# Optimization experiments

Hardware: AMD Instinct MI355X
Metric: run time of the kernel (lower is better)

Reference implementation:

```python
import jax, jax.numpy as jnp
import numpy as np

NINP, NC, NH = 34, 128, 512
B, S, T = 64, 2048, 400
EPS = 1e-10


def _lstm_cell(x, h, c, Wih, Whh, bih, bhh):
    # torch.nn.LSTMCell gate order: i, f, g, o
    g = x @ Wih.T + bih + h @ Whh.T + bhh
    i, f, gg, o = jnp.split(g, 4, axis=1)
    c2 = jax.nn.sigmoid(f) * c + jax.nn.sigmoid(i) * jnp.tanh(gg)
    h2 = jax.nn.sigmoid(o) * jnp.tanh(c2)
    return h2, c2


def _attend(keys, values, mask, query):
    # energy: [B, S]; mask: [B, S] float 0/1
    energy = jnp.einsum('bc,bsc->bs', query, keys) * mask
    energy = energy - (1.0 - mask) * 1e6
    e = jnp.exp(energy - energy.max(axis=1, keepdims=True)) * mask
    att = e / e.sum(axis=1, keepdims=True)
    ctx = jnp.einsum('bs,bsc->bc', att, values)
    return att, ctx


def setup_inputs() -> dict:
    key = jax.random.key(0)
    ks = jax.random.split(key, 32)
    def rn(k, shape, scale=0.05):
        return (jax.random.normal(k, shape) * scale).astype(jnp.float32)
    inp = {
        'keys': rn(ks[0], (B, S, NC), 1.0),
        'values': rn(ks[1], (B, S, NC), 1.0),
        'lens': jax.random.randint(ks[2], (B,), S // 2, S + 1),
        'inputs': jax.random.randint(ks[3], (B, T), 0, NINP),
        'emb': rn(ks[4], (NINP, NC)),
        'wq': rn(ks[5], (NC, NH)), 'bq': jnp.zeros((NC,), jnp.float32),
        'wc': rn(ks[6], (NC, NH + NC)), 'bc': jnp.zeros((NC,), jnp.float32),
        'b_out': jnp.zeros((NINP,), jnp.float32),
    }
    in_sizes = [2 * NC, NH, NH]
    for l in range(3):
        inp['w%d_ih' % l] = rn(ks[7 + 4 * l], (4 * NH, in_sizes[l]))
        inp['w%d_hh' % l] = rn(ks[8 + 4 * l], (4 * NH, NH))
        inp['b%d_ih' % l] = jnp.zeros((4 * NH,), jnp.float32)
        inp['b%d_hh' % l] = jnp.zeros((4 * NH,), jnp.float32)
        inp['h0_%d' % l] = jnp.zeros((NH,), jnp.float32)  # ALSTMCell h0 param (zero init)
        inp['c0_%d' % l] = jnp.zeros((NH,), jnp.float32)
    return inp


def reference(keys, values, lens, inputs, emb, wq, bq, wc, bc, b_out,
              w0_ih, w0_hh, b0_ih, b0_hh, h0_0, c0_0,
              w1_ih, w1_hh, b1_ih, b1_hh, h0_1, c0_1,
              w2_ih, w2_hh, b2_ih, b2_hh, h0_2, c0_2):
    mask = (jnp.arange(S)[None, :] < lens[:, None]).astype(keys.dtype)  # [B,S]
    h1 = jnp.broadcast_to(h0_0[None], (B, NH)); c1 = jnp.broadcast_to(c0_0[None], (B, NH))
    h2 = jnp.broadcast_to(h0_1[None], (B, NH)); c2 = jnp.broadcast_to(c0_1[None], (B, NH))
    h3 = jnp.broadcast_to(h0_2[None], (B, NH)); c3 = jnp.broadcast_to(c0_2[None], (B, NH))
    # initial attention from last layer's h0 (matches torch forward)
    query0 = h3 @ wq.T + bq
    _, ctx = _attend(keys, values, mask, query0)
    # precompute gumbel noise for all T steps: -log(eps - log(U + eps))
    U = jax.random.uniform(jax.random.key(1), (T, B, NINP), dtype=jnp.float32)
    gnoise = -jnp.log(EPS - jnp.log(U + EPS))

    def step(carry, xs):
        h1, c1, h2, c2, h3, c3, ctx = carry
        tok, gn = xs
        x = jnp.concatenate([emb[tok], ctx], axis=1)  # [B, 2*NC]
        h1, c1 = _lstm_cell(x, h1, c1, w0_ih, w0_hh, b0_ih, b0_hh)
        h2, c2 = _lstm_cell(h1, h2, c2, w1_ih, w1_hh, b1_ih, b1_hh)
        h3, c3 = _lstm_cell(h2, h3, c3, w2_ih, w2_hh, b2_ih, b2_hh)
        q = h3 @ wq.T + bq
        att, ctx = _attend(keys, values, mask, q)
        z = jax.nn.leaky_relu(jnp.concatenate([h3, ctx], axis=1) @ wc.T + bc, 0.01)
        logit = z @ emb.T + b_out  # tied output weight = embedding
        gen = jnp.argmax(logit + gn, axis=1)
        return (h1, c1, h2, c2, h3, c3, ctx), (logit, att, gen)

    _, (logits, attentions, generated) = jax.lax.scan(
        step, (h1, c1, h2, c2, h3, c3, ctx), (inputs.T, gnoise))
    return logits, attentions, generated
```

## Files before the change

kernel.cpp:

```cpp
#include <hip/hip_runtime.h>

#define NINP 34
#define NCC  128
#define NHH  512
#define BBB  64
#define SSS  2048
#define TTT  400
#define GEPS 1e-10f

#define GDIM 512
#define NTHR 256
#define NCHK 8
#define SCHK 256

#define JAX_PARTITIONABLE 1

#define OFF_H   0
#define OFF_C   196608
#define OFF_CTX 294912
#define OFF_ML  303104
#define OFF_P   303616

#define SY_ROOT 0
#define SY_GEN  16
#define SY_LEAFC(l) (256 + 8 * (l))
#define SY_LEAFG(l) (512 + 8 * (l))
#define SY_BF(b)    (1024 + 8 * (b))
#define SY_MF(b)    (1536 + 8 * (b))

struct Params {
  const float* keys; const float* values;
  const int* lens;  const int* toks;
  const float* emb; const float* wq; const float* bq;
  const float* wc;  const float* bc; const float* bout;
  const float* wih[3]; const float* whh[3];
  const float* bih[3]; const float* bhh[3];
  const float* h0[3];  const float* c0[3];
  float* out_logits; float* out_att; float* out_gen;
  float* wsf; unsigned* sync;
};

__device__ __forceinline__ float4 ld4(const float* p) { return *(const float4*)p; }
__device__ __forceinline__ float sigf(float x) { return 1.0f / (1.0f + expf(-x)); }

__device__ __forceinline__ unsigned aload(const unsigned* p) {
  return __hip_atomic_load(p, __ATOMIC_RELAXED, __HIP_MEMORY_SCOPE_AGENT);
}
__device__ __forceinline__ unsigned aadd(unsigned* p, unsigned v) {
  return __hip_atomic_fetch_add(p, v, __ATOMIC_RELAXED, __HIP_MEMORY_SCOPE_AGENT);
}
__device__ __forceinline__ void astore(unsigned* p, unsigned v) {
  __hip_atomic_store(p, v, __ATOMIC_RELAXED, __HIP_MEMORY_SCOPE_AGENT);
}
__device__ __forceinline__ float ldc(const float* p) {
  unsigned u = __hip_atomic_load((const unsigned*)p, __ATOMIC_RELAXED, __HIP_MEMORY_SCOPE_AGENT);
  return __uint_as_float(u);
}
__device__ __forceinline__ void stc(float* p, float v) {
  __hip_atomic_store((unsigned*)p, __float_as_uint(v), __ATOMIC_RELAXED, __HIP_MEMORY_SCOPE_AGENT);
}
__device__ __forceinline__ float4 ld4c(const float* p) {
  unsigned long long a = __hip_atomic_load((const unsigned long long*)p,
                                           __ATOMIC_RELAXED, __HIP_MEMORY_SCOPE_AGENT);
  unsigned long long b = __hip_atomic_load(((const unsigned long long*)p) + 1,
                                           __ATOMIC_RELAXED, __HIP_MEMORY_SCOPE_AGENT);
  float4 r;
  r.x = __uint_as_float((unsigned)a); r.y = __uint_as_float((unsigned)(a >> 32));
  r.z = __uint_as_float((unsigned)b); r.w = __uint_as_float((unsigned)(b >> 32));
  return r;
}
__device__ __forceinline__ void wait_vm0() {
  asm volatile("s_waitcnt vmcnt(0)" ::: "memory");
}
__device__ __forceinline__ void cbar() { asm volatile("" ::: "memory"); }

__device__ void gbar(unsigned* sync, unsigned& epoch, int bid) {
  wait_vm0();
  __syncthreads();
  if (threadIdx.x == 0) {
    epoch++;
    const int leaf = bid >> 4;
    const bool leader = (bid & 15) == 0;
    if (aadd(&sync[SY_LEAFC(leaf)], 1u) == 16u * epoch - 1u) {
      if (aadd(&sync[SY_ROOT], 1u) == 32u * epoch - 1u)
        astore(&sync[SY_GEN], epoch);
    }
    if (leader) {
      while (aload(&sync[SY_GEN]) < epoch) __builtin_amdgcn_s_sleep(1);
      astore(&sync[SY_LEAFG(leaf)], epoch);
    } else {
      while (aload(&sync[SY_LEAFG(leaf)]) < epoch) __builtin_amdgcn_s_sleep(1);
    }
  }
  __syncthreads();
  cbar();
}

__device__ __forceinline__ void waitflag(unsigned* p, unsigned target) {
  if (threadIdx.x == 0) {
    while (aload(p) < target) __builtin_amdgcn_s_sleep(2);
  }
  __syncthreads();
  cbar();
}
__device__ __forceinline__ void postflag(unsigned* p) {
  wait_vm0();
  __syncthreads();
  if (threadIdx.x == 0) aadd(p, 1u);
}

__device__ __forceinline__ void tfr(unsigned& x0, unsigned& x1, int r) {
  x0 += x1; x1 = (x1 << r) | (x1 >> (32 - r)); x1 ^= x0;
}
__device__ unsigned threefry_bits(unsigned idx) {
  const unsigned k0 = 0u, k1 = 1u;
  const unsigned k2 = 0x1BD11BDAu ^ k0 ^ k1;
#if JAX_PARTITIONABLE
  unsigned x0 = 0u, x1 = idx;
#else
  const unsigned half = (TTT * BBB * NINP) / 2;
  const bool lo = idx < half;
  unsigned x0 = lo ? idx : idx - half;
  unsigned x1 = lo ? idx + half : idx;
#endif
  x0 += k0; x1 += k1;
  tfr(x0,x1,13); tfr(x0,x1,15); tfr(x0,x1,26); tfr(x0,x1,6);
  x0 += k1; x1 += k2 + 1u;
  tfr(x0,x1,17); tfr(x0,x1,29); tfr(x0,x1,16); tfr(x0,x1,24);
  x0 += k2; x1 += k0 + 2u;
  tfr(x0,x1,13); tfr(x0,x1,15); tfr(x0,x1,26); tfr(x0,x1,6);
  x0 += k0; x1 += k1 + 3u;
  tfr(x0,x1,17); tfr(x0,x1,29); tfr(x0,x1,16); tfr(x0,x1,24);
  x0 += k1; x1 += k2 + 4u;
  tfr(x0,x1,13); tfr(x0,x1,15); tfr(x0,x1,26); tfr(x0,x1,6);
  x0 += k2; x1 += k0 + 5u;
#if JAX_PARTITIONABLE
  return x0 ^ x1;
#else
  return lo ? x0 : x1;
#endif
}
__device__ __forceinline__ float gumbel(unsigned idx) {
  unsigned bits = threefry_bits(idx);
  float u = __uint_as_float((bits >> 9) | 0x3f800000u) - 1.0f;
  u = fmaxf(u, 0.0f);
  return -logf(GEPS - logf(u + GEPS));
}

template<int L>
__device__ void lstm_layer(const Params& p, int t, const float* hin, float* hout,
                           float* sh, int ug, int boct, int tid) {
  const float* hin_l = hin + L * BBB * NHH + (size_t)boct * 8 * NHH;
  float* houtl = hout + L * BBB * NHH;
  float* cl = p.wsf + OFF_C + L * BBB * NHH;
  const float* xlow = (L == 0) ? (const float*)0
                               : (hout + (L - 1) * BBB * NHH + (size_t)boct * 8 * NHH);

  const int insz = (L == 0) ? (2 * NCC) : NHH;
  const int nx = insz >> 7;
  const int nch = nx + 4;

  const int rhat = tid >> 3;
  const int bloc = tid & 7;
  const int g = rhat >> 3, jl = rhat & 7;
  const int j = ug * 8 + jl;
  const int row = g * NHH + j;
  const float* wr  = p.wih[L] + (size_t)row * insz;
  const float* wr2 = p.whh[L] + (size_t)row * NHH;

  float* xb0 = sh;
  float* xb1 = sh + 1056;
  const int kk  = (tid & 31) << 2;
  const int rb0 = tid >> 5;

  float4 pf;
  auto issue = [&](int cc) {
    const int rb = rb0;
    const int gb = boct * 8 + rb;
    const bool isx = cc < nx;
    const int off = (isx ? cc : cc - nx) << 7;
    if (L == 0) {
      if (isx) pf = (cc == 0)
          ? ld4(p.emb + (size_t)p.toks[gb * TTT + t] * NCC + kk)
          : ld4c(p.wsf + OFF_CTX + gb * NCC + kk);
      else pf = ld4c(hin_l + (size_t)rb * NHH + off + kk);
    } else {
      pf = isx ? ld4c(xlow + (size_t)rb * NHH + off + kk)
               : ld4c(hin_l + (size_t)rb * NHH + off + kk);
    }
  };
  auto commit = [&](float* buf) {
    *(float4*)&buf[rb0 * 132 + kk] = pf;
  };

  float acc = p.bih[L][row] + p.bhh[L][row];
  float s0 = 0.f, s1 = 0.f, s2 = 0.f, s3 = 0.f;

  issue(0);
  commit(xb0);
  __syncthreads();
  for (int cc = 0; cc < nch; ++cc) {
    if (cc + 1 < nch) issue(cc + 1);
    const bool isx = cc < nx;
    const int off = (isx ? cc : cc - nx) << 7;
    const float* wp = (isx ? wr : wr2) + off;
    const float* xr = ((cc & 1) ? xb1 : xb0) + bloc * 132;
#pragma unroll 8
    for (int k = 0; k < 128; k += 4) {
      float4 w = ld4(wp + k);
      float4 x = ld4(xr + k);
      s0 = fmaf(w.x, x.x, s0); s1 = fmaf(w.y, x.y, s1);
      s2 = fmaf(w.z, x.z, s2); s3 = fmaf(w.w, x.w, s3);
    }
    if (cc + 1 < nch) commit((cc & 1) ? xb0 : xb1);
    __syncthreads();
  }
  acc += (s0 + s1) + (s2 + s3);

  float* gl = sh + 2112;
  gl[rhat * 8 + bloc] = acc;
  __syncthreads();
  if (tid < 64) {
    const int jl2 = tid >> 3, bl = tid & 7;
    const int b = boct * 8 + bl;
    const int jj = ug * 8 + jl2;
    const float iv = gl[(0  + jl2) * 8 + bl];
    const float fv = gl[(8  + jl2) * 8 + bl];
    const float gv = gl[(16 + jl2) * 8 + bl];
    const float ov = gl[(24 + jl2) * 8 + bl];
    const float cold = cl[(size_t)b * NHH + jj];
    const float cnew = sigf(fv) * cold + sigf(iv) * tanhf(gv);
    const float hnew = sigf(ov) * tanhf(cnew);
    cl[(size_t)b * NHH + jj] = cnew;
    stc(&houtl[(size_t)b * NHH + jj], hnew);
  }
}

__device__ void attend_phase(const Params& p, int a, int t, const float* h3,
                             float* sh, int bid, int tid, bool wout) {
  float* wsf = p.wsf;
  unsigned* sync = p.sync;
  const int b  = (bid & 7) * 8 + (bid >> 6);
  const int ch = (bid >> 3) & 7;
  const int sbase = ch * SCHK;

  float* us  = sh + 8704;
  float* qs  = sh + 9344;
  float* ps  = sh + 9472;
  float* red = sh + 9728;
  float* zs  = sh + 10784;
  float* lg  = sh + 10912;

  if (tid < 128) *(float4*)&us[tid * 4] = ld4c(h3 + (size_t)b * NHH + tid * 4);
  __syncthreads();
  if (tid < NCC) {
    const float* wr = p.wq + (size_t)tid * NHH;
    float s0 = 0.f, s1 = 0.f, s2 = 0.f, s3 = 0.f;
#pragma unroll 8
    for (int k = 0; k < NHH; k += 4) {
      float4 w = ld4(wr + k);
      s0 = fmaf(w.x, us[k],     s0); s1 = fmaf(w.y, us[k + 1], s1);
      s2 = fmaf(w.z, us[k + 2], s2); s3 = fmaf(w.w, us[k + 3], s3);
    }
    qs[tid] = p.bq[tid] + (s0 + s1) + (s2 + s3);
  }
  const int lenb = p.lens[b];
  __syncthreads();

  const int s = sbase + tid;
  const bool msk = s < lenb;
  float e = -1e6f;
  if (msk) {
    const float* kr = p.keys + ((size_t)b * SSS + s) * NCC;
    float e0 = 0.f, e1 = 0.f, e2 = 0.f, e3 = 0.f;
#pragma unroll 8
    for (int c = 0; c < NCC; c += 4) {
      float4 kv = ld4(kr + c);
      e0 = fmaf(qs[c],     kv.x, e0); e1 = fmaf(qs[c + 1], kv.y, e1);
      e2 = fmaf(qs[c + 2], kv.z, e2); e3 = fmaf(qs[c + 3], kv.w, e3);
    }
    e = (e0 + e1) + (e2 + e3);
  }

  float mx = e;
#pragma unroll
  for (int off = 32; off; off >>= 1) mx = fmaxf(mx, __shfl_xor(mx, off));
  if ((tid & 63) == 0) red[tid >> 6] = mx;
  __syncthreads();
  const float mc = fmaxf(fmaxf(red[0], red[1]), fmaxf(red[2], red[3]));
  const float pv = msk ? expf(e - mc) : 0.f;
  ps[tid] = pv;
  float ls = pv;
#pragma unroll
  for (int off = 32; off; off >>= 1) ls += __shfl_xor(ls, off);
  if ((tid & 63) == 0) red[4 + (tid >> 6)] = ls;
  __syncthreads();
  const float lc = (red[4] + red[5]) + (red[6] + red[7]);

  const int c4 = (tid & 31) << 2;
  const int sg = tid >> 5;
  float r0 = 0.f, r1 = 0.f, r2 = 0.f, r3 = 0.f;
  const int nval = min(max(lenb - sbase - sg * 32, 0), 32);
  const float* vb = p.values + ((size_t)b * SSS + sbase + sg * 32) * NCC + c4;
#pragma unroll 4
  for (int i2 = 0; i2 < nval; ++i2) {
    const float pw = ps[sg * 32 + i2];
    float4 vv = ld4(vb + (size_t)i2 * NCC);
    r0 = fmaf(pw, vv.x, r0); r1 = fmaf(pw, vv.y, r1);
    r2 = fmaf(pw, vv.z, r2); r3 = fmaf(pw, vv.w, r3);
  }
  __syncthreads();
  *(float4*)&red[sg * 132 + c4] = make_float4(r0, r1, r2, r3);
  __syncthreads();
  float* pout = wsf + OFF_P + ((size_t)b * NCHK + ch) * 132;
  if (tid < NCC) {
    float sum = 0.f;
#pragma unroll
    for (int sg2 = 0; sg2 < 8; ++sg2) sum += red[sg2 * 132 + tid];
    stc(&pout[2 + tid], sum);
  }
  if (tid == 0) { stc(&pout[0], mc); stc(&pout[1], lc); }
  postflag(&sync[SY_BF(b)]);

  float gm = 0.f, gL = 1.f;
  if (ch == 0) {
    waitflag(&sync[SY_BF(b)], (unsigned)(NCHK * (a + 1)));
    const float* pb = wsf + OFF_P + (size_t)b * NCHK * 132;
    if (tid < 8)       red[tid] = ldc(&pb[tid * 132]);
    else if (tid < 16) red[tid] = ldc(&pb[(tid - 8) * 132 + 1]);
    __syncthreads();
    float m = red[0];
#pragma unroll
    for (int i = 1; i < 8; ++i) m = fmaxf(m, red[i]);
    float L = 0.f;
#pragma unroll
    for (int i = 0; i < 8; ++i) L += red[8 + i] * expf(red[i] - m);
    gm = m; gL = L;
    if (tid < NCC) {
      float v = 0.f;
#pragma unroll
      for (int c2 = 0; c2 < NCHK; ++c2)
        v += ldc(&pb[c2 * 132 + 2 + tid]) * expf(red[c2] - m);
      v /= L;
      stc(&wsf[OFF_CTX + b * NCC + tid], v);
      us[NHH + tid] = v;
    }
    if (tid == 0) { stc(&wsf[OFF_ML + b * 8], m); stc(&wsf[OFF_ML + b * 8 + 1], L); }
    postflag(&sync[SY_MF(b)]);
  } else if (wout) {
    waitflag(&sync[SY_MF(b)], (unsigned)(a + 1));
    gm = ldc(&wsf[OFF_ML + b * 8]);
    gL = ldc(&wsf[OFF_ML + b * 8 + 1]);
  }

  if (wout) {
    float* ao = p.out_att + ((size_t)t * BBB + b) * SSS;
    ao[s] = (msk ? expf(e - gm) : 0.f) / gL;
    if (ch == 0) {
      if (tid < NCC) {
        const float* wr = p.wc + (size_t)tid * (NHH + NCC);
        float s0 = 0.f, s1 = 0.f, s2 = 0.f, s3 = 0.f;
#pragma unroll 8
        for (int k = 0; k < NHH + NCC; k += 4) {
          float4 w = ld4(wr + k);
          s0 = fmaf(w.x, us[k],     s0); s1 = fmaf(w.y, us[k + 1], s1);
          s2 = fmaf(w.z, us[k + 2], s2); s3 = fmaf(w.w, us[k + 3], s3);
        }
        float z = (s0 + s1) + (s2 + s3) + p.bc[tid];
        zs[tid] = (z >= 0.f) ? z : 0.01f * z;
      }
      __syncthreads();
      if (tid < NINP) {
        const float* er = p.emb + tid * NCC;
        float s0 = 0.f, s1 = 0.f, s2 = 0.f, s3 = 0.f;
#pragma unroll 8
        for (int k = 0; k < NCC; k += 4) {
          float4 w = ld4(er + k);
          s0 = fmaf(w.x, zs[k],     s0); s1 = fmaf(w.y, zs[k + 1], s1);
          s2 = fmaf(w.z, zs[k + 2], s2); s3 = fmaf(w.w, zs[k + 3], s3);
        }
        const float lgt = (s0 + s1) + (s2 + s3) + p.bout[tid];
        p.out_logits[((size_t)t * BBB + b) * NINP + tid] = lgt;
        lg[tid] = lgt + gumbel((unsigned)(t * (BBB * NINP) + b * NINP + tid));
      }
      __syncthreads();
      if (tid == 0) {
        float bv = lg[0]; int bix = 0;
        for (int i = 1; i < NINP; ++i) if (lg[i] > bv) { bv = lg[i]; bix = i; }
        p.out_gen[t * BBB + b] = (float)bix;
      }
      __syncthreads();
    }
  }
}

extern "C" __global__ void __launch_bounds__(NTHR, 2)
decoder_kernel(Params p) {
  __shared__ float sh[11008];
  const int bid = blockIdx.x;
  const int tid = threadIdx.x;
  const int ug   = (bid & 7) * 8 + ((bid >> 3) & 7);
  const int boct = bid >> 6;
  unsigned epoch = 0;
  unsigned* sync = p.sync;
  float* wsf = p.wsf;

  if (tid < 192) {
    const int l = tid >> 6, u = tid & 63;
    const int jl = u >> 3, bl = u & 7;
    const int b = boct * 8 + bl;
    const int j = ug * 8 + jl;
    stc(&wsf[OFF_H + ((size_t)l * BBB + b) * NHH + j], p.h0[l][j]);
    wsf[OFF_C + ((size_t)l * BBB + b) * NHH + j] = p.c0[l][j];
  }
  gbar(sync, epoch, bid);

  attend_phase(p, 0, -1, wsf + OFF_H + 2 * BBB * NHH, sh, bid, tid, false);
  gbar(sync, epoch, bid);

  for (int t = 0; t < TTT; ++t) {
    const float* hin = wsf + OFF_H + ((t & 1) ? 3 * BBB * NHH : 0);
    float* hout      = wsf + OFF_H + ((t & 1) ? 0 : 3 * BBB * NHH);

    lstm_layer<0>(p, t, hin, hout, sh, ug, boct, tid);
    gbar(sync, epoch, bid);
    lstm_layer<1>(p, t, hin, hout, sh, ug, boct, tid);
    gbar(sync, epoch, bid);
    lstm_layer<2>(p, t, hin, hout, sh, ug, boct, tid);
    gbar(sync, epoch, bid);
    attend_phase(p, t + 1, t, hout + 2 * BBB * NHH, sh, bid, tid, true);
    gbar(sync, epoch, bid);
  }
}

extern "C" void kernel_launch(void* const* d_in, const int* in_sizes, int n_in,
                              void* d_out, int out_size, void* d_ws, size_t ws_size,
                              hipStream_t stream) {
  Params p;
  p.keys   = (const float*)d_in[0];
  p.values = (const float*)d_in[1];
  p.lens   = (const int*)d_in[2];
  p.toks   = (const int*)d_in[3];
  p.emb    = (const float*)d_in[4];
  p.wq     = (const float*)d_in[5];
  p.bq     = (const float*)d_in[6];
  p.wc     = (const float*)d_in[7];
  p.bc     = (const float*)d_in[8];
  p.bout   = (const float*)d_in[9];
  for (int l = 0; l < 3; ++l) {
    p.wih[l] = (const float*)d_in[10 + 6 * l];
    p.whh[l] = (const float*)d_in[11 + 6 * l];
    p.bih[l] = (const float*)d_in[12 + 6 * l];
    p.bhh[l] = (const float*)d_in[13 + 6 * l];
    p.h0[l]  = (const float*)d_in[14 + 6 * l];
    p.c0[l]  = (const float*)d_in[15 + 6 * l];
  }
  float* out = (float*)d_out;
  p.out_logits = out;
  p.out_att    = out + (size_t)TTT * BBB * NINP;
  p.out_gen    = out + (size_t)TTT * BBB * NINP + (size_t)TTT * BBB * SSS;
  p.sync = (unsigned*)d_ws;
  p.wsf  = (float*)((char*)d_ws + 8192);

  hipMemsetAsync(d_ws, 0, 8192, stream);
  decoder_kernel<<<dim3(GDIM), dim3(NTHR), 0, stream>>>(p);
}
```

Measured before the change: 43.23 ms.

## Precompute recurrent Whh·h partials off the critical path of LSTM layers

Restructures the per-step schedule so each layer's recurrent product Whh·h(t) is computed as soon as h is produced. Layer L+1 reuses its staged input to also compute Whh[L]·h_L, and the attention phase computes Whh[2]·h3 plus the next token's embedding term. This shrinks the serialized work between grid barriers: layer 0 does only the ctx part, and layers 1 and 2 do a single shared input pass. The h buffers are no longer double-buffered, and the attention chunk assignment is rotated, adding register state and extra work in the attention phase.

```diff
diff --git a/kernel.cpp b/kernel.cpp
--- a/kernel.cpp
+++ b/kernel.cpp
@@ -147,75 +147,126 @@
   return -logf(GEPS - logf(u + GEPS));
 }
 
+__device__ float pc_dot_h(const float* hsrc, const float* wrow, float* sh, int tid) {
+  float* xb0 = sh;
+  const int kk = (tid & 31) << 2;
+  const int rb0 = tid >> 5;
+  const int bloc = tid & 7;
+  float s0 = 0.f, s1 = 0.f, s2 = 0.f, s3 = 0.f;
+  for (int cc = 0; cc < 4; ++cc) {
+    __syncthreads();
+    *(float4*)&xb0[rb0 * 132 + kk] = ld4c(hsrc + (size_t)rb0 * NHH + (cc << 7) + kk);
+    __syncthreads();
+    const float* xr = xb0 + bloc * 132;
+    const float* wp = wrow + (cc << 7);
+#pragma unroll 8
+    for (int k = 0; k < 128; k += 4) {
+      float4 w = ld4(wp + k);
+      float4 x = ld4(xr + k);
+      s0 = fmaf(w.x, x.x, s0); s1 = fmaf(w.y, x.y, s1);
+      s2 = fmaf(w.z, x.z, s2); s3 = fmaf(w.w, x.w, s3);
+    }
+  }
+  return (s0 + s1) + (s2 + s3);
+}
+
+__device__ float pc_dot_emb(const Params& p, int tnext, const float* wrow,
+                            float* sh, int boct, int tid) {
+  float* xb0 = sh;
+  const int kk = (tid & 31) << 2;
+  const int rb0 = tid >> 5;
+  const int bloc = tid & 7;
+  const int gb = boct * 8 + rb0;
+  __syncthreads();
+  *(float4*)&xb0[rb0 * 132 + kk] =
+      ld4(p.emb + (size_t)p.toks[gb * TTT + tnext] * NCC + kk);
+  __syncthreads();
+  const float* xr = xb0 + bloc * 132;
+  float s0 = 0.f, s1 = 0.f, s2 = 0.f, s3 = 0.f;
+#pragma unroll 8
+  for (int k = 0; k < 128; k += 4) {
+    float4 w = ld4(wrow + k);
+    float4 x = ld4(xr + k);
+    s0 = fmaf(w.x, x.x, s0); s1 = fmaf(w.y, x.y, s1);
+    s2 = fmaf(w.z, x.z, s2); s3 = fmaf(w.w, x.w, s3);
+  }
+  return (s0 + s1) + (s2 + s3);
+}
+
 template<int L>
-__device__ void lstm_layer(const Params& p, int t, const float* hin, float* hout,
-                           float* sh, int ug, int boct, int tid) {
-  const float* hin_l = hin + L * BBB * NHH + (size_t)boct * 8 * NHH;
+__device__ void lstm_layer(const Params& p, float* hout, float* sh, int ug, int boct,
+                           int tid, float use_hacc, float embacc, float* prod_hacc) {
   float* houtl = hout + L * BBB * NHH;
   float* cl = p.wsf + OFF_C + L * BBB * NHH;
-  const float* xlow = (L == 0) ? (const float*)0
+  const float* xsrc = (L == 0) ? (const float*)0
                                : (hout + (L - 1) * BBB * NHH + (size_t)boct * 8 * NHH);
-
-  const int insz = (L == 0) ? (2 * NCC) : NHH;
-  const int nx = insz >> 7;
-  const int nch = nx + 4;
 
   const int rhat = tid >> 3;
   const int bloc = tid & 7;
   const int g = rhat >> 3, jl = rhat & 7;
   const int j = ug * 8 + jl;
   const int row = g * NHH + j;
-  const float* wr  = p.wih[L] + (size_t)row * insz;
-  const float* wr2 = p.whh[L] + (size_t)row * NHH;
+  constexpr int insz = (L == 0) ? (2 * NCC) : NHH;
+  const float* wx = p.wih[L] + (size_t)row * insz + ((L == 0) ? NCC : 0);
+  const float* wh = (L == 0) ? (const float*)0 : (p.whh[L - 1] + (size_t)row * NHH);
 
   float* xb0 = sh;
   float* xb1 = sh + 1056;
-  const int kk  = (tid & 31) << 2;
+  const int kk = (tid & 31) << 2;
   const int rb0 = tid >> 5;
+  const int gb = boct * 8 + rb0;
+  constexpr int nch = (L == 0) ? 1 : 4;
+
+  float xs0 = 0.f, xs1 = 0.f, xs2 = 0.f, xs3 = 0.f;
+  float hs0 = 0.f, hs1 = 0.f, hs2 = 0.f, hs3 = 0.f;
 
   float4 pf;
   auto issue = [&](int cc) {
-    const int rb = rb0;
-    const int gb = boct * 8 + rb;
-    const bool isx = cc < nx;
-    const int off = (isx ? cc : cc - nx) << 7;
-    if (L == 0) {
-      if (isx) pf = (cc == 0)
-          ? ld4(p.emb + (size_t)p.toks[gb * TTT + t] * NCC + kk)
-          : ld4c(p.wsf + OFF_CTX + gb * NCC + kk);
-      else pf = ld4c(hin_l + (size_t)rb * NHH + off + kk);
+    if constexpr (L == 0) {
+      (void)cc;
+      pf = ld4c(p.wsf + OFF_CTX + gb * NCC + kk);
     } else {
-      pf = isx ? ld4c(xlow + (size_t)rb * NHH + off + kk)
-               : ld4c(hin_l + (size_t)rb * NHH + off + kk);
+      pf = ld4c(xsrc + (size_t)rb0 * NHH + (cc << 7) + kk);
     }
   };
-  auto commit = [&](float* buf) {
-    *(float4*)&buf[rb0 * 132 + kk] = pf;
-  };
-
-  float acc = p.bih[L][row] + p.bhh[L][row];
-  float s0 = 0.f, s1 = 0.f, s2 = 0.f, s3 = 0.f;
+  auto commit = [&](float* buf) { *(float4*)&buf[rb0 * 132 + kk] = pf; };
 
   issue(0);
   commit(xb0);
   __syncthreads();
   for (int cc = 0; cc < nch; ++cc) {
     if (cc + 1 < nch) issue(cc + 1);
-    const bool isx = cc < nx;
-    const int off = (isx ? cc : cc - nx) << 7;
-    const float* wp = (isx ? wr : wr2) + off;
+    const int off = cc << 7;
     const float* xr = ((cc & 1) ? xb1 : xb0) + bloc * 132;
-#pragma unroll 8
-    for (int k = 0; k < 128; k += 4) {
-      float4 w = ld4(wp + k);
-      float4 x = ld4(xr + k);
-      s0 = fmaf(w.x, x.x, s0); s1 = fmaf(w.y, x.y, s1);
-      s2 = fmaf(w.z, x.z, s2); s3 = fmaf(w.w, x.w, s3);
+    const float* wp = wx + off;
+    if constexpr (L == 0) {
+#pragma unroll 8
+      for (int k = 0; k < 128; k += 4) {
+        float4 w = ld4(wp + k);
+        float4 x = ld4(xr + k);
+        xs0 = fmaf(w.x, x.x, xs0); xs1 = fmaf(w.y, x.y, xs1);
+        xs2 = fmaf(w.z, x.z, xs2); xs3 = fmaf(w.w, x.w, xs3);
+      }
+    } else {
+      const float* wp2 = wh + off;
+#pragma unroll 8
+      for (int k = 0; k < 128; k += 4) {
+        float4 x = ld4(xr + k);
+        float4 w = ld4(wp + k);
+        xs0 = fmaf(w.x, x.x, xs0); xs1 = fmaf(w.y, x.y, xs1);
+        xs2 = fmaf(w.z, x.z, xs2); xs3 = fmaf(w.w, x.w, xs3);
+        float4 w2 = ld4(wp2 + k);
+        hs0 = fmaf(w2.x, x.x, hs0); hs1 = fmaf(w2.y, x.y, hs1);
+        hs2 = fmaf(w2.z, x.z, hs2); hs3 = fmaf(w2.w, x.w, hs3);
+      }
     }
     if (cc + 1 < nch) commit((cc & 1) ? xb0 : xb1);
     __syncthreads();
   }
-  acc += (s0 + s1) + (s2 + s3);
+  if constexpr (L > 0) *prod_hacc = (hs0 + hs1) + (hs2 + hs3);
+
+  float acc = p.bih[L][row] + p.bhh[L][row] + (xs0 + xs1) + (xs2 + xs3) + use_hacc;
+  if constexpr (L == 0) acc += embacc;
 
   float* gl = sh + 2112;
   gl[rhat * 8 + bloc] = acc;
@@ -237,12 +288,13 @@
 }
 
 __device__ void attend_phase(const Params& p, int a, int t, const float* h3,
-                             float* sh, int bid, int tid, bool wout) {
+                             float* sh, int bid, int tid, bool wout,
+                             int ug, int boct, int pc_t, float* hacc2, float* embacc) {
   float* wsf = p.wsf;
   unsigned* sync = p.sync;
   const int b  = (bid & 7) * 8 + (bid >> 6);
   const int ch = (bid >> 3) & 7;
-  const int sbase = ch * SCHK;
+  const int sbase = ((ch + 7) & 7) * SCHK;
 
   float* us  = sh + 8704;
   float* qs  = sh + 9344;
@@ -322,7 +374,11 @@
   if (tid == 0) { stc(&pout[0], mc); stc(&pout[1], lc); }
   postflag(&sync[SY_BF(b)]);
 
-  float gm = 0.f, gL = 1.f;
+  const int rowp = ((tid >> 3) >> 3) * NHH + (ug * 8 + ((tid >> 3) & 7));
+  const float* wh2row = p.whh[2] + (size_t)rowp * NHH;
+  const float* w0row  = p.wih[0] + (size_t)rowp * (2 * NCC);
+  const float* h3pc   = p.wsf + OFF_H + 2 * BBB * NHH + (size_t)boct * 8 * NHH;
+
   if (ch == 0) {
     waitflag(&sync[SY_BF(b)], (unsigned)(NCHK * (a + 1)));
     const float* pb = wsf + OFF_P + (size_t)b * NCHK * 132;
@@ -335,7 +391,6 @@
     float L = 0.f;
 #pragma unroll
     for (int i = 0; i < 8; ++i) L += red[8 + i] * expf(red[i] - m);
-    gm = m; gL = L;
     if (tid < NCC) {
       float v = 0.f;
 #pragma unroll
@@ -347,16 +402,14 @@
     }
     if (tid == 0) { stc(&wsf[OFF_ML + b * 8], m); stc(&wsf[OFF_ML + b * 8 + 1], L); }
     postflag(&sync[SY_MF(b)]);
-  } else if (wout) {
-    waitflag(&sync[SY_MF(b)], (unsigned)(a + 1));
-    gm = ldc(&wsf[OFF_ML + b * 8]);
-    gL = ldc(&wsf[OFF_ML + b * 8 + 1]);
-  }
-
-  if (wout) {
-    float* ao = p.out_att + ((size_t)t * BBB + b) * SSS;
-    ao[s] = (msk ? expf(e - gm) : 0.f) / gL;
-    if (ch == 0) {
+
+    if (pc_t >= 0) {
+      *hacc2  = pc_dot_h(h3pc, wh2row, sh, tid);
+      *embacc = pc_dot_emb(p, pc_t, w0row, sh, boct, tid);
+    }
+    if (wout) {
+      float* ao = p.out_att + ((size_t)t * BBB + b) * SSS;
+      ao[s] = (msk ? expf(e - m) : 0.f) / L;
       if (tid < NCC) {
         const float* wr = p.wc + (size_t)tid * (NHH + NCC);
         float s0 = 0.f, s1 = 0.f, s2 = 0.f, s3 = 0.f;
@@ -391,6 +444,18 @@
       }
       __syncthreads();
     }
+  } else {
+    if (pc_t >= 0) {
+      *hacc2  = pc_dot_h(h3pc, wh2row, sh, tid);
+      *embacc = pc_dot_emb(p, pc_t, w0row, sh, boct, tid);
+    }
+    if (wout) {
+      waitflag(&sync[SY_MF(b)], (unsigned)(a + 1));
+      const float gm = ldc(&wsf[OFF_ML + b * 8]);
+      const float gL = ldc(&wsf[OFF_ML + b * 8 + 1]);
+      float* ao = p.out_att + ((size_t)t * BBB + b) * SSS;
+      ao[s] = (msk ? expf(e - gm) : 0.f) / gL;
+    }
   }
 }
 
@@ -404,31 +469,43 @@
   unsigned epoch = 0;
   unsigned* sync = p.sync;
   float* wsf = p.wsf;
+  float* hbuf = wsf + OFF_H;
 
   if (tid < 192) {
     const int l = tid >> 6, u = tid & 63;
     const int jl = u >> 3, bl = u & 7;
     const int b = boct * 8 + bl;
     const int j = ug * 8 + jl;
-    stc(&wsf[OFF_H + ((size_t)l * BBB + b) * NHH + j], p.h0[l][j]);
+    stc(&hbuf[((size_t)l * BBB + b) * NHH + j], p.h0[l][j]);
     wsf[OFF_C + ((size_t)l * BBB + b) * NHH + j] = p.c0[l][j];
   }
   gbar(sync, epoch, bid);
 
-  attend_phase(p, 0, -1, wsf + OFF_H + 2 * BBB * NHH, sh, bid, tid, false);
+  float hacc0, hacc1, hacc2, embacc;
+  {
+    const int rowp = ((tid >> 3) >> 3) * NHH + (ug * 8 + ((tid >> 3) & 7));
+    hacc0 = pc_dot_h(hbuf + 0 * BBB * NHH + (size_t)boct * 8 * NHH,
+                     p.whh[0] + (size_t)rowp * NHH, sh, tid);
+    hacc1 = pc_dot_h(hbuf + 1 * BBB * NHH + (size_t)boct * 8 * NHH,
+                     p.whh[1] + (size_t)rowp * NHH, sh, tid);
+    hacc2 = pc_dot_h(hbuf + 2 * BBB * NHH + (size_t)boct * 8 * NHH,
+                     p.whh[2] + (size_t)rowp * NHH, sh, tid);
+    embacc = pc_dot_emb(p, 0, p.wih[0] + (size_t)rowp * (2 * NCC), sh, boct, tid);
+  }
+
+  attend_phase(p, 0, -1, hbuf + 2 * BBB * NHH, sh, bid, tid, false,
+               ug, boct, -1, &hacc2, &embacc);
   gbar(sync, epoch, bid);
 
   for (int t = 0; t < TTT; ++t) {
-    const float* hin = wsf + OFF_H + ((t & 1) ? 3 * BBB * NHH : 0);
-    float* hout      = wsf + OFF_H + ((t & 1) ? 0 : 3 * BBB * NHH);
-
-    lstm_layer<0>(p, t, hin, hout, sh, ug, boct, tid);
+    lstm_layer<0>(p, hbuf, sh, ug, boct, tid, hacc0, embacc, (float*)0);
     gbar(sync, epoch, bid);
-    lstm_layer<1>(p, t, hin, hout, sh, ug, boct, tid);
+    lstm_layer<1>(p, hbuf, sh, ug, boct, tid, hacc1, 0.f, &hacc0);
     gbar(sync, epoch, bid);
-    lstm_layer<2>(p, t, hin, hout, sh, ug, boct, tid);
+    lstm_layer<2>(p, hbuf, sh, ug, boct, tid, hacc2, 0.f, &hacc1);
     gbar(sync, epoch, bid);
-    attend_phase(p, t + 1, t, hout + 2 * BBB * NHH, sh, bid, tid, true);
+    attend_phase(p, t + 1, t, hbuf + 2 * BBB * NHH, sh, bid, tid, true,
+                 ug, boct, (t + 1 < TTT) ? (t + 1) : -1, &hacc2, &embacc);
     gbar(sync, epoch, bid);
   }
 }
```

Result: slower. 46.86 ms (+8.4%).
